# Performance work log

Hardware: AMD Instinct MI355X
Metric: run time of the kernel (lower is better)

Reference implementation:

```python
import jax, jax.numpy as jnp
import numpy as np

B, S, DK, H = 4, 4096, 768, 64

def setup_inputs() -> dict:
    key = jax.random.key(0)
    ks = jax.random.split(key, 5)
    scale = 1.0 / np.sqrt(DK)
    x = jax.random.normal(ks[0], (B, S, DK), dtype=jnp.float32)
    Wq = jax.random.normal(ks[1], (H, DK), dtype=jnp.float32) * scale
    bq = jnp.zeros((H,), dtype=jnp.float32)
    Wv = jax.random.normal(ks[2], (H, DK), dtype=jnp.float32) * scale
    bv = jnp.zeros((H,), dtype=jnp.float32)
    return {"x": x, "Wq": Wq, "bq": bq, "Wv": Wv, "bv": bv}

def reference(x, Wq, bq, Wv, bv):
    # Faithful to source: k uses the QUERY projection (source bug), scale = d_k**-0.5 with d_k = input dim
    dk = x.shape[-1]
    q = jnp.einsum('bsd,hd->bsh', x, Wq) + bq  # [B,S,H]
    k = jnp.einsum('bsd,hd->bsh', x, Wq) + bq  # same projection as q
    v = jnp.einsum('bsd,hd->bsh', x, Wv) + bv
    score = jnp.einsum('bqh,bkh->bqk', q, k) * (dk ** -0.5)  # [B,S,S]
    prob = jax.nn.softmax(score, axis=-1)
    out = jnp.einsum('bqk,bkh->bqh', prob, v)  # [B,S,H]
    return out
```

## Files before the change

kernel.cpp:

```cpp
#include <hip/hip_runtime.h>
#include <hip/hip_bf16.h>
#include <stdint.h>
#include <math.h>


typedef unsigned short u16;
typedef __attribute__((ext_vector_type(8))) short bf16x8;
typedef __attribute__((ext_vector_type(4))) float f32x4;

#define MFMA16(a,b,c) __builtin_amdgcn_mfma_f32_16x16x32_bf16((a),(b),(c),0,0,0)

__device__ __forceinline__ u16 f2bf(float f) {
  union { float f; uint32_t u; } v; v.f = f;
  uint32_t u = v.u;
  return (u16)((u + 0x7FFFu + ((u >> 16) & 1u)) >> 16);
}

__device__ __forceinline__ bf16x8 ldsfrag(const u16* lds, int row, int k) {
  return *(const bf16x8*)(lds + row * 64 + (k ^ ((row & 7) << 3)));
}

__device__ __forceinline__ void gload_lds16(const void* g, void* l) {
  __builtin_amdgcn_global_load_lds(
      (__attribute__((address_space(1))) void*)g,
      (__attribute__((address_space(3))) void*)l, 16, 0, 0);
}

__global__ __launch_bounds__(256) void proj_k(
    const float* __restrict__ x, const float* __restrict__ Wq,
    const float* __restrict__ bq, const float* __restrict__ Wv,
    const float* __restrict__ bv, u16* __restrict__ qbf,
    u16* __restrict__ vtbf, float qscale)
{
  __shared__ __align__(16) u16 xs[64 * 64];
  __shared__ __align__(16) u16 wqs[64 * 64];
  __shared__ __align__(16) u16 wvs[64 * 64];
  const int tid = threadIdx.x;
  const int lane = tid & 63;
  const int w = tid >> 6;
  const int l15 = lane & 15, lg = lane >> 4;
  const int s0 = blockIdx.x * 64;

  f32x4 acc[2][4];
#pragma unroll
  for (int i = 0; i < 2; i++)
#pragma unroll
    for (int n = 0; n < 4; n++) acc[i][n] = (f32x4){0.f, 0.f, 0.f, 0.f};

  const int srow = tid >> 2;
  const int scol = (tid & 3) << 4;

  for (int ks = 0; ks < 12; ++ks) {
    const int k0 = ks << 6;
    if (ks) __syncthreads();
    {
      const float* srcs[3] = { x + (size_t)(s0 + srow) * 768 + k0 + scol,
                               Wq + (size_t)srow * 768 + k0 + scol,
                               Wv + (size_t)srow * 768 + k0 + scol };
      u16* tiles[3] = { xs, wqs, wvs };
#pragma unroll
      for (int tset = 0; tset < 3; ++tset) {
        const float4* s4 = (const float4*)srcs[tset];
        float4 a = s4[0], b = s4[1], c = s4[2], d = s4[3];
        bf16x8 lo, hi;
        lo[0] = (short)f2bf(a.x); lo[1] = (short)f2bf(a.y);
        lo[2] = (short)f2bf(a.z); lo[3] = (short)f2bf(a.w);
        lo[4] = (short)f2bf(b.x); lo[5] = (short)f2bf(b.y);
        lo[6] = (short)f2bf(b.z); lo[7] = (short)f2bf(b.w);
        hi[0] = (short)f2bf(c.x); hi[1] = (short)f2bf(c.y);
        hi[2] = (short)f2bf(c.z); hi[3] = (short)f2bf(c.w);
        hi[4] = (short)f2bf(d.x); hi[5] = (short)f2bf(d.y);
        hi[6] = (short)f2bf(d.z); hi[7] = (short)f2bf(d.w);
        const int xsw = (srow & 7) << 3;
        *(bf16x8*)(tiles[tset] + srow * 64 + (scol ^ xsw)) = lo;
        *(bf16x8*)(tiles[tset] + srow * 64 + ((scol + 8) ^ xsw)) = hi;
      }
    }
    __syncthreads();
#pragma unroll
    for (int kk = 0; kk < 2; ++kk) {
      const int k = kk * 32 + lg * 8;
      if (w < 2) {
        bf16x8 a0 = ldsfrag(xs, (2 * w + 0) * 16 + l15, k);
        bf16x8 a1 = ldsfrag(xs, (2 * w + 1) * 16 + l15, k);
#pragma unroll
        for (int n = 0; n < 4; n++) {
          bf16x8 bb = ldsfrag(wqs, n * 16 + l15, k);
          acc[0][n] = MFMA16(a0, bb, acc[0][n]);
          acc[1][n] = MFMA16(a1, bb, acc[1][n]);
        }
      } else {
        bf16x8 a0 = ldsfrag(wvs, (2 * (w - 2) + 0) * 16 + l15, k);
        bf16x8 a1 = ldsfrag(wvs, (2 * (w - 2) + 1) * 16 + l15, k);
#pragma unroll
        for (int n = 0; n < 4; n++) {
          bf16x8 bb = ldsfrag(xs, n * 16 + l15, k);
          acc[0][n] = MFMA16(a0, bb, acc[0][n]);
          acc[1][n] = MFMA16(a1, bb, acc[1][n]);
        }
      }
    }
  }

  if (w < 2) {
#pragma unroll
    for (int i = 0; i < 2; i++)
#pragma unroll
      for (int n = 0; n < 4; n++) {
        const int h = n * 16 + l15;
        const float bias = bq[h];
#pragma unroll
        for (int r = 0; r < 4; r++) {
          const int sg = s0 + (2 * w + i) * 16 + lg * 4 + r;
          qbf[(size_t)sg * 64 + h] = f2bf((acc[i][n][r] + bias) * qscale);
        }
      }
  } else {
    const int b = s0 >> 12;
    const int sloc = s0 & 4095;
#pragma unroll
    for (int i = 0; i < 2; i++)
#pragma unroll
      for (int n = 0; n < 4; n++) {
        const int scg = sloc + n * 16 + l15;
#pragma unroll
        for (int r = 0; r < 4; r++) {
          const int h = (2 * (w - 2) + i) * 16 + lg * 4 + r;
          vtbf[(size_t)(b * 64 + h) * 4096 + scg] = f2bf(acc[i][n][r] + bv[h]);
        }
      }
  }
}

__global__ __launch_bounds__(512) void attn_k(
    const u16* __restrict__ qbf, const u16* __restrict__ vtbf,
    float* __restrict__ out)
{
  __shared__ __align__(16) u16 smem[8192 + 8192 + 8 * 640];
  u16* kt0 = smem;
  u16* vt0 = smem + 8192;
  u16* pl  = smem + 16384;
  const int tid = threadIdx.x;
  const int lane = tid & 63;
  const int w = tid >> 6;
  const int wq = w & 3, wk = w >> 2;
  const int l15 = lane & 15, lg = lane >> 4;
  const int b = blockIdx.y;
  const int q0 = blockIdx.x << 6;

  bf16x8 qf[2];
  {
    const u16* qr = qbf + (size_t)(b * 4096 + q0 + wq * 16 + l15) * 64 + lg * 8;
    qf[0] = *(const bf16x8*)(qr);
    qf[1] = *(const bf16x8*)(qr + 32);
  }

  f32x4 oacc[4];
#pragma unroll
  for (int i = 0; i < 4; i++) oacc[i] = (f32x4){0.f, 0.f, 0.f, 0.f};
  float lacc[4] = {0.f, 0.f, 0.f, 0.f};

  const int o = tid << 4;
  const int krow = o >> 7;
  const int ksw = o ^ ((krow & 7) << 4);
  const char* kbase = (const char*)qbf + (size_t)(b * 4096) * 128;
  const char* vbase = (const char*)vtbf + (size_t)(b * 64 + krow) * 8192 + (ksw & 127);
  char* ldst_k = (char*)kt0 + w * 1024;
  char* ldst_v = (char*)vt0 + w * 1024;

  const int NT = 64;
  gload_lds16(kbase + ksw, ldst_k);
  gload_lds16(vbase, ldst_v);

  for (int t = 0; t < NT; ++t) {
    const int buf = t & 1;
    __syncthreads();
    if (t + 1 < NT) {
      const int nb = (t + 1) & 1;
      gload_lds16(kbase + (size_t)(t + 1) * 8192 + ksw, ldst_k + nb * 8192);
      gload_lds16(vbase + (t + 1) * 128, ldst_v + nb * 8192);
    }
    const u16* kt = kt0 + buf * 4096;
    const u16* vt = vt0 + buf * 4096;

    f32x4 sc0 = (f32x4){0.f, 0.f, 0.f, 0.f}, sc1 = sc0;
#pragma unroll
    for (int j = 0; j < 2; j++) {
      const int dk = j * 32 + lg * 8;
      bf16x8 k0f = ldsfrag(kt, wk * 32 + l15, dk);
      bf16x8 k1f = ldsfrag(kt, wk * 32 + 16 + l15, dk);
      sc0 = MFMA16(qf[j], k0f, sc0);
      sc1 = MFMA16(qf[j], k1f, sc1);
    }
    float p0[4], p1[4], rs[4];
#pragma unroll
    for (int r = 0; r < 4; r++) {
      p0[r] = __expf(sc0[r]);
      p1[r] = __expf(sc1[r]);
      rs[r] = p0[r] + p1[r];
    }
#pragma unroll
    for (int m = 1; m < 16; m <<= 1)
#pragma unroll
      for (int r = 0; r < 4; r++) rs[r] += __shfl_xor(rs[r], m, 64);
#pragma unroll
    for (int r = 0; r < 4; r++) lacc[r] += rs[r];
    u16* pw = pl + w * 640;
#pragma unroll
    for (int r = 0; r < 4; r++) {
      pw[(lg * 4 + r) * 40 + l15]      = f2bf(p0[r]);
      pw[(lg * 4 + r) * 40 + 16 + l15] = f2bf(p1[r]);
    }
    asm volatile("s_waitcnt lgkmcnt(0)" ::: "memory");
    bf16x8 pf = *(const bf16x8*)(pw + l15 * 40 + lg * 8);
#pragma unroll
    for (int db = 0; db < 4; ++db) {
      bf16x8 vf = ldsfrag(vt, db * 16 + l15, wk * 32 + lg * 8);
      oacc[db] = MFMA16(pf, vf, oacc[db]);
    }
  }

  __syncthreads();
  float* oc = (float*)smem;
  float* lc = oc + 4 * 16 * 68;
  if (wk == 1) {
#pragma unroll
    for (int db = 0; db < 4; ++db)
#pragma unroll
      for (int r = 0; r < 4; r++)
        oc[(wq * 16 + lg * 4 + r) * 68 + db * 16 + l15] = oacc[db][r];
#pragma unroll
    for (int r = 0; r < 4; r++) lc[wq * 16 + lg * 4 + r] = lacc[r];
  }
  __syncthreads();
  if (wk == 0) {
#pragma unroll
    for (int db = 0; db < 4; ++db)
#pragma unroll
      for (int r = 0; r < 4; r++) {
        const int row = lg * 4 + r;
        const float ov = oacc[db][r] + oc[(wq * 16 + row) * 68 + db * 16 + l15];
        const float lt = lacc[r] + lc[wq * 16 + row];
        out[(size_t)(b * 4096 + q0 + wq * 16 + row) * 64 + db * 16 + l15] = ov / lt;
      }
  }
}

extern "C" void kernel_launch(void* const* d_in, const int* in_sizes, int n_in,
                              void* d_out, int out_size, void* d_ws, size_t ws_size,
                              hipStream_t stream) {
  const float* x  = (const float*)d_in[0];
  const float* Wq = (const float*)d_in[1];
  const float* bq = (const float*)d_in[2];
  const float* Wv = (const float*)d_in[3];
  const float* bv = (const float*)d_in[4];
  float* out = (float*)d_out;
  u16* qbf  = (u16*)d_ws;
  u16* vtbf = qbf + (size_t)16384 * 64;
  const float qscale = 1.0f / sqrtf(sqrtf(768.0f));
  proj_k<<<dim3(256), dim3(256), 0, stream>>>(x, Wq, bq, Wv, bv, qbf, vtbf, qscale);
  attn_k<<<dim3(64, 4), dim3(512), 0, stream>>>(qbf, vtbf, out);
}
```

Measured before the change: 167.4 us.

## Software-pipeline projection loads and triple-buffer attention K/V staging

The projection kernel now double-buffers its LDS tiles and issues global loads into registers two k-steps ahead, converting and storing the next tile after the MFMAs, so there is one barrier per step instead of two. The attention kernel moves from double to triple buffering, with explicit vmcnt waits and raw s_barrier, so tiles are prefetched two iterations ahead. It also raises wave priority around MFMA sections. This adds register and LDS pressure, and hand-counted vmcnt values could break correctness if the compiler reorders loads.

Result: no change. 165.6 us (-1.1%).

```diff
diff --git a/kernel.cpp b/kernel.cpp
--- a/kernel.cpp
+++ b/kernel.cpp
@@ -24,6 +24,40 @@
   __builtin_amdgcn_global_load_lds(
       (__attribute__((address_space(1))) void*)g,
       (__attribute__((address_space(3))) void*)l, 16, 0, 0);
+}
+
+struct Regs { float4 r[12]; };
+
+__device__ __forceinline__ void issue_loads(Regs& R, const float* xp,
+                                            const float* qp, const float* vp,
+                                            int ks) {
+  const float4* a = (const float4*)(xp + (ks << 6));
+  const float4* b = (const float4*)(qp + (ks << 6));
+  const float4* c = (const float4*)(vp + (ks << 6));
+  R.r[0] = a[0]; R.r[1] = a[1]; R.r[2] = a[2]; R.r[3] = a[3];
+  R.r[4] = b[0]; R.r[5] = b[1]; R.r[6] = b[2]; R.r[7] = b[3];
+  R.r[8] = c[0]; R.r[9] = c[1]; R.r[10] = c[2]; R.r[11] = c[3];
+}
+
+__device__ __forceinline__ void cvt8(const float4& a, const float4& b, bf16x8& o) {
+  o[0] = (short)f2bf(a.x); o[1] = (short)f2bf(a.y);
+  o[2] = (short)f2bf(a.z); o[3] = (short)f2bf(a.w);
+  o[4] = (short)f2bf(b.x); o[5] = (short)f2bf(b.y);
+  o[6] = (short)f2bf(b.z); o[7] = (short)f2bf(b.w);
+}
+
+__device__ __forceinline__ void cvt_store(const Regs& R, u16* xrow, u16* qrow,
+                                          u16* vrow, int scol, int xsw) {
+  bf16x8 lo, hi;
+  cvt8(R.r[0], R.r[1], lo);  cvt8(R.r[2], R.r[3], hi);
+  *(bf16x8*)(xrow + (scol ^ xsw)) = lo;
+  *(bf16x8*)(xrow + ((scol + 8) ^ xsw)) = hi;
+  cvt8(R.r[4], R.r[5], lo);  cvt8(R.r[6], R.r[7], hi);
+  *(bf16x8*)(qrow + (scol ^ xsw)) = lo;
+  *(bf16x8*)(qrow + ((scol + 8) ^ xsw)) = hi;
+  cvt8(R.r[8], R.r[9], lo);  cvt8(R.r[10], R.r[11], hi);
+  *(bf16x8*)(vrow + (scol ^ xsw)) = lo;
+  *(bf16x8*)(vrow + ((scol + 8) ^ xsw)) = hi;
 }
 
 __global__ __launch_bounds__(256) void proj_k(
@@ -32,9 +66,9 @@
     const float* __restrict__ bv, u16* __restrict__ qbf,
     u16* __restrict__ vtbf, float qscale)
 {
-  __shared__ __align__(16) u16 xs[64 * 64];
-  __shared__ __align__(16) u16 wqs[64 * 64];
-  __shared__ __align__(16) u16 wvs[64 * 64];
+  __shared__ __align__(16) u16 xs[2][4096];
+  __shared__ __align__(16) u16 wqs[2][4096];
+  __shared__ __align__(16) u16 wvs[2][4096];
   const int tid = threadIdx.x;
   const int lane = tid & 63;
   const int w = tid >> 6;
@@ -49,56 +83,62 @@
 
   const int srow = tid >> 2;
   const int scol = (tid & 3) << 4;
-
+  const int xsw = (srow & 7) << 3;
+  const float* xsrc = x + (size_t)(s0 + srow) * 768 + scol;
+  const float* qsrc = Wq + (size_t)srow * 768 + scol;
+  const float* vsrc = Wv + (size_t)srow * 768 + scol;
+
+  Regs A, B;
+  issue_loads(A, xsrc, qsrc, vsrc, 0);
+  issue_loads(B, xsrc, qsrc, vsrc, 1);
+  asm volatile("s_waitcnt vmcnt(12)" ::: "memory");
+  cvt_store(A, &xs[0][srow * 64], &wqs[0][srow * 64], &wvs[0][srow * 64], scol, xsw);
+
+#pragma unroll
   for (int ks = 0; ks < 12; ++ks) {
-    const int k0 = ks << 6;
-    if (ks) __syncthreads();
-    {
-      const float* srcs[3] = { x + (size_t)(s0 + srow) * 768 + k0 + scol,
-                               Wq + (size_t)srow * 768 + k0 + scol,
-                               Wv + (size_t)srow * 768 + k0 + scol };
-      u16* tiles[3] = { xs, wqs, wvs };
-#pragma unroll
-      for (int tset = 0; tset < 3; ++tset) {
-        const float4* s4 = (const float4*)srcs[tset];
-        float4 a = s4[0], b = s4[1], c = s4[2], d = s4[3];
-        bf16x8 lo, hi;
-        lo[0] = (short)f2bf(a.x); lo[1] = (short)f2bf(a.y);
-        lo[2] = (short)f2bf(a.z); lo[3] = (short)f2bf(a.w);
-        lo[4] = (short)f2bf(b.x); lo[5] = (short)f2bf(b.y);
-        lo[6] = (short)f2bf(b.z); lo[7] = (short)f2bf(b.w);
-        hi[0] = (short)f2bf(c.x); hi[1] = (short)f2bf(c.y);
-        hi[2] = (short)f2bf(c.z); hi[3] = (short)f2bf(c.w);
-        hi[4] = (short)f2bf(d.x); hi[5] = (short)f2bf(d.y);
-        hi[6] = (short)f2bf(d.z); hi[7] = (short)f2bf(d.w);
-        const int xsw = (srow & 7) << 3;
-        *(bf16x8*)(tiles[tset] + srow * 64 + (scol ^ xsw)) = lo;
-        *(bf16x8*)(tiles[tset] + srow * 64 + ((scol + 8) ^ xsw)) = hi;
-      }
-    }
-    __syncthreads();
+    const int b = ks & 1;
+    if (ks + 2 < 12) {
+      if (b) issue_loads(B, xsrc, qsrc, vsrc, ks + 2);
+      else   issue_loads(A, xsrc, qsrc, vsrc, ks + 2);
+    }
+    asm volatile("s_waitcnt lgkmcnt(0)" ::: "memory");
+    __builtin_amdgcn_s_barrier();
+    __builtin_amdgcn_sched_barrier(0);
+
+    const u16* xt = xs[b];
+    const u16* qt = wqs[b];
+    const u16* vt = wvs[b];
 #pragma unroll
     for (int kk = 0; kk < 2; ++kk) {
       const int k = kk * 32 + lg * 8;
       if (w < 2) {
-        bf16x8 a0 = ldsfrag(xs, (2 * w + 0) * 16 + l15, k);
-        bf16x8 a1 = ldsfrag(xs, (2 * w + 1) * 16 + l15, k);
+        bf16x8 a0 = ldsfrag(xt, (2 * w + 0) * 16 + l15, k);
+        bf16x8 a1 = ldsfrag(xt, (2 * w + 1) * 16 + l15, k);
 #pragma unroll
         for (int n = 0; n < 4; n++) {
-          bf16x8 bb = ldsfrag(wqs, n * 16 + l15, k);
+          bf16x8 bb = ldsfrag(qt, n * 16 + l15, k);
           acc[0][n] = MFMA16(a0, bb, acc[0][n]);
           acc[1][n] = MFMA16(a1, bb, acc[1][n]);
         }
       } else {
-        bf16x8 a0 = ldsfrag(wvs, (2 * (w - 2) + 0) * 16 + l15, k);
-        bf16x8 a1 = ldsfrag(wvs, (2 * (w - 2) + 1) * 16 + l15, k);
+        bf16x8 a0 = ldsfrag(vt, (2 * (w - 2) + 0) * 16 + l15, k);
+        bf16x8 a1 = ldsfrag(vt, (2 * (w - 2) + 1) * 16 + l15, k);
 #pragma unroll
         for (int n = 0; n < 4; n++) {
-          bf16x8 bb = ldsfrag(xs, n * 16 + l15, k);
+          bf16x8 bb = ldsfrag(xt, n * 16 + l15, k);
           acc[0][n] = MFMA16(a0, bb, acc[0][n]);
           acc[1][n] = MFMA16(a1, bb, acc[1][n]);
         }
       }
+    }
+    if (ks + 1 < 12) {
+      if (ks < 10) asm volatile("s_waitcnt vmcnt(12)" ::: "memory");
+      else         asm volatile("s_waitcnt vmcnt(0)" ::: "memory");
+      u16* xd = &xs[b ^ 1][srow * 64];
+      u16* qd = &wqs[b ^ 1][srow * 64];
+      u16* vd = &wvs[b ^ 1][srow * 64];
+      if (b) cvt_store(A, xd, qd, vd, scol, xsw);
+      else   cvt_store(B, xd, qd, vd, scol, xsw);
     }
   }
 
@@ -136,10 +176,8 @@
     const u16* __restrict__ qbf, const u16* __restrict__ vtbf,
     float* __restrict__ out)
 {
-  __shared__ __align__(16) u16 smem[8192 + 8192 + 8 * 640];
-  u16* kt0 = smem;
-  u16* vt0 = smem + 8192;
-  u16* pl  = smem + 16384;
+  __shared__ __align__(16) u16 smem[3 * 8192 + 8 * 640];
+  u16* pl = smem + 3 * 8192;
   const int tid = threadIdx.x;
   const int lane = tid & 63;
   const int w = tid >> 6;
@@ -165,25 +203,30 @@
   const int ksw = o ^ ((krow & 7) << 4);
   const char* kbase = (const char*)qbf + (size_t)(b * 4096) * 128;
   const char* vbase = (const char*)vtbf + (size_t)(b * 64 + krow) * 8192 + (ksw & 127);
-  char* ldst_k = (char*)kt0 + w * 1024;
-  char* ldst_v = (char*)vt0 + w * 1024;
 
   const int NT = 64;
-  gload_lds16(kbase + ksw, ldst_k);
-  gload_lds16(vbase, ldst_v);
-
+  auto stage = [&](int t, int s3) {
+    char* kd = (char*)smem + s3 * 16384 + o;
+    gload_lds16(kbase + (size_t)t * 8192 + ksw, kd);
+    gload_lds16(vbase + t * 128, kd + 8192);
+  };
+
+  stage(0, 0);
+  stage(1, 1);
+
+  int sl = 0, sp = 2;
   for (int t = 0; t < NT; ++t) {
-    const int buf = t & 1;
-    __syncthreads();
-    if (t + 1 < NT) {
-      const int nb = (t + 1) & 1;
-      gload_lds16(kbase + (size_t)(t + 1) * 8192 + ksw, ldst_k + nb * 8192);
-      gload_lds16(vbase + (t + 1) * 128, ldst_v + nb * 8192);
-    }
-    const u16* kt = kt0 + buf * 4096;
-    const u16* vt = vt0 + buf * 4096;
+    if (t < NT - 1) asm volatile("s_waitcnt vmcnt(2)" ::: "memory");
+    else            asm volatile("s_waitcnt vmcnt(0)" ::: "memory");
+    __builtin_amdgcn_s_barrier();
+    __builtin_amdgcn_sched_barrier(0);
+    if (t + 2 < NT) stage(t + 2, sp);
+
+    const u16* kt = smem + sl * 8192;
+    const u16* vt = kt + 4096;
 
     f32x4 sc0 = (f32x4){0.f, 0.f, 0.f, 0.f}, sc1 = sc0;
+    __builtin_amdgcn_s_setprio(1);
 #pragma unroll
     for (int j = 0; j < 2; j++) {
       const int dk = j * 32 + lg * 8;
@@ -192,6 +235,7 @@
       sc0 = MFMA16(qf[j], k0f, sc0);
       sc1 = MFMA16(qf[j], k1f, sc1);
     }
+    __builtin_amdgcn_s_setprio(0);
     float p0[4], p1[4], rs[4];
 #pragma unroll
     for (int r = 0; r < 4; r++) {
@@ -213,11 +257,16 @@
     }
     asm volatile("s_waitcnt lgkmcnt(0)" ::: "memory");
     bf16x8 pf = *(const bf16x8*)(pw + l15 * 40 + lg * 8);
+    __builtin_amdgcn_s_setprio(1);
 #pragma unroll
     for (int db = 0; db < 4; ++db) {
       bf16x8 vf = ldsfrag(vt, db * 16 + l15, wk * 32 + lg * 8);
       oacc[db] = MFMA16(pf, vf, oacc[db]);
     }
+    __builtin_amdgcn_s_setprio(0);
+
+    sl = (sl == 2) ? 0 : sl + 1;
+    sp = (sp == 2) ? 0 : sp + 1;
   }
 
   __syncthreads();
```
